# Kernel optimization log

Measured on AMD Instinct MI355X. Metric: run time of the kernel, lower is better.

## Reference

```python
import jax, jax.numpy as jnp
import numpy as np

B, L, H, V = 32, 2048, 128, 32000
ALPHA = 0.95
GATE_THRESH = 0.7
LN_EPS = 1e-5
NORM_EPS = 1e-12


def setup_inputs() -> dict:
    key = jax.random.key(0)
    ks = jax.random.split(key, 12)
    s = 0.02
    return {
        "seq": jax.random.randint(ks[0], (B, L), 0, V),
        "embed_w": jax.random.normal(ks[1], (V, H), jnp.float32) * s,
        "ff_w1": jax.random.normal(ks[2], (2 * H, H), jnp.float32) * s,
        "ff_b1": jnp.zeros((2 * H,), jnp.float32),
        "ff_w2": jax.random.normal(ks[3], (H, 2 * H), jnp.float32) * s,
        "ff_b2": jnp.zeros((H,), jnp.float32),
        "ln_g": jnp.ones((H,), jnp.float32),
        "ln_b": jnp.zeros((H,), jnp.float32),
        "kp_w": jax.random.normal(ks[4], (H, H), jnp.float32) * s,
        "rp_w": jax.random.normal(ks[5], (H, H), jnp.float32) * s,
        "rp_b": jnp.zeros((H,), jnp.float32),
        "out_w": jax.random.normal(ks[6], (V, H), jnp.float32) * s,
        "out_b": jnp.zeros((V,), jnp.float32),
    }


def reference(seq, embed_w, ff_w1, ff_b1, ff_w2, ff_b2, ln_g, ln_b,
              kp_w, rp_w, rp_b, out_w, out_b):
    h = embed_w[seq]                                    # (B,L,H)
    ff = jnp.maximum(h @ ff_w1.T + ff_b1, 0.0) @ ff_w2.T + ff_b2
    x = h + ff
    mu = jnp.mean(x, axis=-1, keepdims=True)
    var = jnp.mean((x - mu) ** 2, axis=-1, keepdims=True)
    h = (x - mu) * jax.lax.rsqrt(var + LN_EPS) * ln_g + ln_b

    k_all = jnp.einsum('blh,oh->blo', h, kp_w)          # kp(h), (B,L,H)
    ks_seq = jnp.transpose(k_all[:, :-1, :], (1, 0, 2)) # (L-1,B,H)

    def step(M, k):
        kn = k / jnp.maximum(jnp.linalg.norm(k, axis=-1, keepdims=True), NORM_EPS)
        vp = jnp.einsum('bij,bj->bi', M, kn)
        err = k - vp
        fire = (jnp.linalg.norm(err, axis=-1)
                >= GATE_THRESH * jnp.linalg.norm(k, axis=-1)).astype(k.dtype)
        delta = fire[:, None, None] * err[:, :, None] * kn[:, None, :]
        return M + (1.0 - ALPHA) * delta, None

    M0 = jnp.zeros((B, H, H), h.dtype)
    M, _ = jax.lax.scan(step, M0, ks_seq)

    q = k_all[:, -1, :]                                 # (B,H)
    read = jnp.einsum('bij,bj->bi', M, q)
    r = read @ rp_w.T + rp_b
    return r @ out_w.T + out_b                          # (B,V)
```

## Files before the change

kernel.cpp:

```cpp
#include <hip/hip_runtime.h>
#include <hip/hip_fp16.h>

#define B_  32
#define L_  2048
#define H_  128
#define H2_ 256
#define V_  32000
#define NT_ (B_*L_)
#define TOKS_PER_BLK 64
#define CH_ 32

template<int CTRL, int RMASK>
__device__ __forceinline__ float dpp_add(float x) {
    int v = __builtin_amdgcn_update_dpp(0, __float_as_int(x), CTRL, RMASK, 0xf, true);
    return x + __int_as_float(v);
}
__device__ __forceinline__ float wave_sum63(float x) {
    x = dpp_add<0x111, 0xf>(x);
    x = dpp_add<0x112, 0xf>(x);
    x = dpp_add<0x114, 0xf>(x);
    x = dpp_add<0x118, 0xf>(x);
    x = dpp_add<0x142, 0xa>(x);
    x = dpp_add<0x143, 0xc>(x);
    return x;
}
__device__ __forceinline__ float wave_allsum(float x) {
    x = wave_sum63(x);
    return __int_as_float(__builtin_amdgcn_readlane(__float_as_int(x), 63));
}
__device__ __forceinline__ float pair_sum(float x) {
    int v = __builtin_amdgcn_update_dpp(0, __float_as_int(x), 0xB1, 0xf, 0xf, true);
    return x + __int_as_float(v);
}

__global__ __launch_bounds__(256, 2) void ka_ff_ln_kp(
    const int*   __restrict__ seq,   const float* __restrict__ embed_w,
    const float* __restrict__ ff_w1, const float* __restrict__ ff_b1,
    const float* __restrict__ ff_w2, const float* __restrict__ ff_b2,
    const float* __restrict__ ln_g,  const float* __restrict__ ln_b,
    const float* __restrict__ kp_w,  float* __restrict__ k_all)
{
    __shared__ __half2 w1p[64][256];
    __shared__ float2 h2[128];
    __shared__ float2 y12[256];
    __shared__ float  p_sh[2][2][128];
    __shared__ float2 hln2[128];
    __shared__ float  red_sh[8];

    const int tid  = threadIdx.x;
    const int half = tid >> 7;
    const int i    = tid & 127;
    const int lane = tid & 63;
    const int wave = tid >> 6;

    for (int idx = tid; idx < 64*256; idx += 256) {
        int o = idx >> 6, j2 = idx & 63;
        float2 ab = *(const float2*)(ff_w1 + o*128 + 2*j2);
        w1p[j2][o] = __floats2half2_rn(ab.x, ab.y);
    }
    __half2 w2r[64];
    {
        const float* src = ff_w2 + (size_t)i*H2_ + half*128;
        #pragma unroll
        for (int q4 = 0; q4 < 16; ++q4) {
            float4 a = *(const float4*)(src + q4*8);
            float4 b = *(const float4*)(src + q4*8 + 4);
            w2r[q4*4+0] = __floats2half2_rn(a.x, a.y);
            w2r[q4*4+1] = __floats2half2_rn(a.z, a.w);
            w2r[q4*4+2] = __floats2half2_rn(b.x, b.y);
            w2r[q4*4+3] = __floats2half2_rn(b.z, b.w);
        }
    }
    float kreg[64];
    {
        const float* src = kp_w + (size_t)i*H_ + half*64;
        #pragma unroll
        for (int j4 = 0; j4 < 16; ++j4) {
            float4 v = *(const float4*)(src + j4*4);
            kreg[j4*4+0]=v.x; kreg[j4*4+1]=v.y; kreg[j4*4+2]=v.z; kreg[j4*4+3]=v.w;
        }
    }
    const float b1v = ff_b1[tid];
    const float b2v = ff_b2[i];
    const float gv  = ln_g[i];
    const float bv  = ln_b[i];
    __syncthreads();

    const int base = blockIdx.x * TOKS_PER_BLK;
    for (int it = 0; it < TOKS_PER_BLK; it += 2) {
        const int t0 = base + it;
        if (tid < 64) {
            int tok = tid >> 5;
            int l32 = tid & 31;
            int v   = seq[t0 + tok];
            float4 hv = *(const float4*)(embed_w + (size_t)v*H_ + l32*4);
            ((float*)&h2[l32*4+0])[tok] = hv.x;
            ((float*)&h2[l32*4+1])[tok] = hv.y;
            ((float*)&h2[l32*4+2])[tok] = hv.z;
            ((float*)&h2[l32*4+3])[tok] = hv.w;
        }
        __syncthreads();
        float a0 = b1v, a1 = b1v;
        #pragma unroll
        for (int j2 = 0; j2 < 64; ++j2) {
            __half2 w = w1p[j2][tid];
            float4 hh = *(const float4*)&h2[2*j2];
            float wl = __low2float(w), wh = __high2float(w);
            a0 = fmaf(wl, hh.x, a0); a0 = fmaf(wh, hh.z, a0);
            a1 = fmaf(wl, hh.y, a1); a1 = fmaf(wh, hh.w, a1);
        }
        y12[tid] = make_float2(fmaxf(a0, 0.f), fmaxf(a1, 0.f));
        __syncthreads();
        float c0 = 0.f, c1 = 0.f;
        #pragma unroll
        for (int q = 0; q < 64; ++q) {
            __half2 w = w2r[q];
            float4 yy = *(const float4*)&y12[half*128 + 2*q];
            float wl = __low2float(w), wh = __high2float(w);
            c0 = fmaf(wl, yy.x, c0); c0 = fmaf(wh, yy.z, c0);
            c1 = fmaf(wl, yy.y, c1); c1 = fmaf(wh, yy.w, c1);
        }
        p_sh[half][0][i] = c0;
        p_sh[half][1][i] = c1;
        __syncthreads();
        float x = ((const float*)&h2[i])[half] + p_sh[0][half][i] + p_sh[1][half][i] + b2v;
        {
            float s = x, s2 = x*x;
            #pragma unroll
            for (int m = 1; m <= 32; m <<= 1) {
                s  += __shfl_xor(s,  m);
                s2 += __shfl_xor(s2, m);
            }
            if (lane == 0) { red_sh[wave*2] = s; red_sh[wave*2+1] = s2; }
        }
        __syncthreads();
        float mu  = (red_sh[half*4+0] + red_sh[half*4+2]) * (1.0f/128.0f);
        float ex2 = (red_sh[half*4+1] + red_sh[half*4+3]) * (1.0f/128.0f);
        float var = ex2 - mu*mu;
        float rstd = 1.0f / sqrtf(var + 1e-5f);
        float hln = (x - mu) * rstd * gv + bv;
        ((float*)&hln2[i])[half] = hln;
        __syncthreads();
        float k0 = 0.f, k1 = 0.f;
        #pragma unroll
        for (int jj = 0; jj < 64; ++jj) {
            float2 hh = hln2[half*64 + jj];
            k0 = fmaf(kreg[jj], hh.x, k0);
            k1 = fmaf(kreg[jj], hh.y, k1);
        }
        p_sh[half][0][i] = k0;
        p_sh[half][1][i] = k1;
        __syncthreads();
        if (tid < 128) {
            k_all[(size_t)t0*H_     + i] = p_sh[0][0][i] + p_sh[1][0][i];
            k_all[(size_t)(t0+1)*H_ + i] = p_sh[0][1][i] + p_sh[1][1][i];
        }
    }
}

__global__ __launch_bounds__(256, 1) void kc_scan(
    const float* __restrict__ k_all, const float* __restrict__ rp_w,
    const float* __restrict__ rp_b,  float* __restrict__ r_out)
{
    __shared__ __align__(16) float kch[2][CH_*H_];
    __shared__ __align__(16) float red[2][4];
    __shared__ __align__(16) float read_sh[128];
    __shared__ float pr_sh[2][128];

    const int b    = blockIdx.x;
    const int tid  = threadIdx.x;
    const int lane = tid & 63;
    const int wave = tid >> 6;
    const int half = lane & 1;
    const int r    = wave*32 + (lane >> 1);

    const float* kb = k_all + (size_t)b * (L_*H_);

    float M[64];
    #pragma unroll
    for (int j = 0; j < 64; ++j) M[j] = 0.f;

    #pragma unroll
    for (int jr = 0; jr < 4; ++jr) {
        float4 v = *(const float4*)(kb + jr*1024 + tid*4);
        *(float4*)&kch[0][jr*1024 + tid*4] = v;
    }
    float4 st[4];
    __syncthreads();

    #pragma unroll 1
    for (int t = 0; t < L_-1; ++t) {
        const int c   = t >> 5;
        const int row = t & 31;
        const int buf = c & 1;
        if (row == 0 && c + 1 < L_/CH_) {
            const float* src = kb + (size_t)(c+1)*(CH_*H_);
            #pragma unroll
            for (int jr = 0; jr < 4; ++jr) st[jr] = *(const float4*)(src + jr*1024 + tid*4);
        }
        if (row == 16 && c + 1 < L_/CH_) {
            float* dst = &kch[buf^1][0];
            #pragma unroll
            for (int jr = 0; jr < 4; ++jr) *(float4*)&dst[jr*1024 + tid*4] = st[jr];
        }
        const float* krow = &kch[buf][row*H_];
        float2 kq = *(const float2*)(krow + (lane<<1));
        float nk2 = wave_allsum(fmaf(kq.x, kq.x, kq.y*kq.y));
        float rn  = 1.0f / fmaxf(sqrtf(nk2), 1e-12f);
        float K[64];
        float a0=0.f, a1=0.f, a2=0.f, a3=0.f;
        #pragma unroll
        for (int j4 = 0; j4 < 16; ++j4) {
            float4 kk = *(const float4*)(krow + half*64 + j4*4);
            K[j4*4+0]=kk.x; K[j4*4+1]=kk.y; K[j4*4+2]=kk.z; K[j4*4+3]=kk.w;
            a0 = fmaf(M[j4*4+0], kk.x, a0);
            a1 = fmaf(M[j4*4+1], kk.y, a1);
            a2 = fmaf(M[j4*4+2], kk.z, a2);
            a3 = fmaf(M[j4*4+3], kk.w, a3);
        }
        float vp = pair_sum((a0+a1) + (a2+a3));
        float kr  = krow[r];
        float err = kr - vp*rn;
        float esum = wave_sum63(err*err);
        if (lane == 63) red[t&1][wave] = esum;
        __syncthreads();
        float4 rv = *(const float4*)&red[t&1][0];
        float ne2x2 = (rv.x+rv.y) + (rv.z+rv.w);
        int fire = ne2x2 >= 0.98f * nk2;
        if (__builtin_amdgcn_readfirstlane(fire)) {
            float sc = 0.05f * err * rn;
            #pragma unroll
            for (int j = 0; j < 64; ++j) M[j] = fmaf(sc, K[j], M[j]);
        }
    }

    {
        const float* qrow = &kch[1][31*H_];
        float a0=0.f, a1=0.f, a2=0.f, a3=0.f;
        #pragma unroll
        for (int j4 = 0; j4 < 16; ++j4) {
            float4 kk = *(const float4*)(qrow + half*64 + j4*4);
            a0 = fmaf(M[j4*4+0], kk.x, a0);
            a1 = fmaf(M[j4*4+1], kk.y, a1);
            a2 = fmaf(M[j4*4+2], kk.z, a2);
            a3 = fmaf(M[j4*4+3], kk.w, a3);
        }
        float vq = pair_sum((a0+a1) + (a2+a3));
        if (half == 0) read_sh[r] = vq;
    }
    __syncthreads();
    {
        const int o  = tid & 127;
        const int hf = tid >> 7;
        float acc = 0.f;
        #pragma unroll
        for (int j4 = 0; j4 < 16; ++j4) {
            float4 wv = *(const float4*)(rp_w + (size_t)o*H_ + hf*64 + j4*4);
            float4 rv = *(const float4*)&read_sh[hf*64 + j4*4];
            acc = fmaf(wv.x, rv.x, acc);
            acc = fmaf(wv.y, rv.y, acc);
            acc = fmaf(wv.z, rv.z, acc);
            acc = fmaf(wv.w, rv.w, acc);
        }
        pr_sh[hf][o] = acc;
    }
    __syncthreads();
    if (tid < 128) r_out[b*H_ + tid] = pr_sh[0][tid] + pr_sh[1][tid] + rp_b[tid];
}

__global__ __launch_bounds__(256) void kd_out(
    const float* __restrict__ r_in, const float* __restrict__ out_w,
    const float* __restrict__ out_b, float* __restrict__ out)
{
    __shared__ float r_sh[B_ * H_];
    const int tid = threadIdx.x;
    for (int idx = tid; idx < B_*H_; idx += 256) r_sh[idx] = r_in[idx];
    __syncthreads();
    const int v = blockIdx.x * 256 + tid;
    const float* wrow = out_w + (size_t)v * H_;
    float acc[B_];
    #pragma unroll
    for (int bb = 0; bb < B_; ++bb) acc[bb] = 0.f;
    for (int h4 = 0; h4 < H_/4; ++h4) {
        float4 w = *(const float4*)(wrow + h4*4);
        #pragma unroll
        for (int bb = 0; bb < B_; ++bb) {
            const float* rr = &r_sh[bb*H_ + h4*4];
            acc[bb] = fmaf(w.x, rr[0], acc[bb]);
            acc[bb] = fmaf(w.y, rr[1], acc[bb]);
            acc[bb] = fmaf(w.z, rr[2], acc[bb]);
            acc[bb] = fmaf(w.w, rr[3], acc[bb]);
        }
    }
    const float bias = out_b[v];
    #pragma unroll
    for (int bb = 0; bb < B_; ++bb) out[(size_t)bb*V_ + v] = acc[bb] + bias;
}

extern "C" void kernel_launch(void* const* d_in, const int* in_sizes, int n_in,
                              void* d_out, int out_size, void* d_ws, size_t ws_size,
                              hipStream_t stream)
{
    const int*   seq     = (const int*)  d_in[0];
    const float* embed_w = (const float*)d_in[1];
    const float* ff_w1   = (const float*)d_in[2];
    const float* ff_b1   = (const float*)d_in[3];
    const float* ff_w2   = (const float*)d_in[4];
    const float* ff_b2   = (const float*)d_in[5];
    const float* ln_g    = (const float*)d_in[6];
    const float* ln_b    = (const float*)d_in[7];
    const float* kp_w    = (const float*)d_in[8];
    const float* rp_w    = (const float*)d_in[9];
    const float* rp_b    = (const float*)d_in[10];
    const float* out_w   = (const float*)d_in[11];
    const float* out_b   = (const float*)d_in[12];
    float* out = (float*)d_out;

    float* k_all = (float*)d_ws;
    float* r_buf = k_all + (size_t)NT_ * H_;

    ka_ff_ln_kp<<<dim3(NT_/TOKS_PER_BLK), dim3(256), 0, stream>>>(
        seq, embed_w, ff_w1, ff_b1, ff_w2, ff_b2, ln_g, ln_b, kp_w, k_all);
    kc_scan<<<dim3(B_), dim3(256), 0, stream>>>(k_all, rp_w, rp_b, r_buf);
    kd_out<<<dim3(V_/256), dim3(256), 0, stream>>>(r_buf, out_w, out_b, out);
}
```

Measured before the change: 1.938 ms.

## Restructure scan with lagged rank-1 update and fdot2 FFN matvecs

The scan loop is restructured so that each step applies the previous step's rank-1 update to M while computing M·k for the next key. The current prediction is corrected algebraically using the dot product between consecutive keys, which removes the separate update pass and the data dependency from the serial critical path. The chunk prefetch and store are rescheduled, and the per-column half rotation is meant to reduce LDS bank conflicts. The feed-forward kernel switches to packed fp16 activations with the fdot2 builtin, which cuts instruction count but adds rounding of activations to half precision.

Result: slower. 2.171 ms (+12.0%).

```diff
diff --git a/kernel.cpp b/kernel.cpp
--- a/kernel.cpp
+++ b/kernel.cpp
@@ -10,6 +10,16 @@
 #define TOKS_PER_BLK 64
 #define CH_ 32
 
+typedef _Float16 h2v __attribute__((ext_vector_type(2)));
+
+__device__ __forceinline__ float fdot2f(h2v a, h2v b, float c) {
+#if __has_builtin(__builtin_amdgcn_fdot2)
+    return __builtin_amdgcn_fdot2(a, b, c, false);
+#else
+    return fmaf((float)a[1], (float)b[1], fmaf((float)a[0], (float)b[0], c));
+#endif
+}
+
 template<int CTRL, int RMASK>
 __device__ __forceinline__ float dpp_add(float x) {
     int v = __builtin_amdgcn_update_dpp(0, __float_as_int(x), CTRL, RMASK, 0xf, true);
@@ -40,9 +50,10 @@
     const float* __restrict__ ln_g,  const float* __restrict__ ln_b,
     const float* __restrict__ kp_w,  float* __restrict__ k_all)
 {
-    __shared__ __half2 w1p[64][256];
+    __shared__ h2v w1p[64][256];
     __shared__ float2 h2[128];
-    __shared__ float2 y12[256];
+    __shared__ h2v   h16[2][64];
+    __shared__ _Float16 y16[2][256];
     __shared__ float  p_sh[2][2][128];
     __shared__ float2 hln2[128];
     __shared__ float  red_sh[8];
@@ -56,19 +67,17 @@
     for (int idx = tid; idx < 64*256; idx += 256) {
         int o = idx >> 6, j2 = idx & 63;
         float2 ab = *(const float2*)(ff_w1 + o*128 + 2*j2);
-        w1p[j2][o] = __floats2half2_rn(ab.x, ab.y);
-    }
-    __half2 w2r[64];
+        h2v p; p[0] = (_Float16)ab.x; p[1] = (_Float16)ab.y;
+        w1p[j2][o] = p;
+    }
+    h2v w2r[64];
     {
         const float* src = ff_w2 + (size_t)i*H2_ + half*128;
         #pragma unroll
-        for (int q4 = 0; q4 < 16; ++q4) {
-            float4 a = *(const float4*)(src + q4*8);
-            float4 b = *(const float4*)(src + q4*8 + 4);
-            w2r[q4*4+0] = __floats2half2_rn(a.x, a.y);
-            w2r[q4*4+1] = __floats2half2_rn(a.z, a.w);
-            w2r[q4*4+2] = __floats2half2_rn(b.x, b.y);
-            w2r[q4*4+3] = __floats2half2_rn(b.z, b.w);
+        for (int q2 = 0; q2 < 64; ++q2) {
+            float2 ab = *(const float2*)(src + 2*q2);
+            h2v p; p[0] = (_Float16)ab.x; p[1] = (_Float16)ab.y;
+            w2r[q2] = p;
         }
     }
     float kreg[64];
@@ -98,27 +107,28 @@
             ((float*)&h2[l32*4+1])[tok] = hv.y;
             ((float*)&h2[l32*4+2])[tok] = hv.z;
             ((float*)&h2[l32*4+3])[tok] = hv.w;
+            h2v pa; pa[0]=(_Float16)hv.x; pa[1]=(_Float16)hv.y;
+            h2v pb; pb[0]=(_Float16)hv.z; pb[1]=(_Float16)hv.w;
+            h16[tok][l32*2+0] = pa;
+            h16[tok][l32*2+1] = pb;
         }
         __syncthreads();
         float a0 = b1v, a1 = b1v;
         #pragma unroll
         for (int j2 = 0; j2 < 64; ++j2) {
-            __half2 w = w1p[j2][tid];
-            float4 hh = *(const float4*)&h2[2*j2];
-            float wl = __low2float(w), wh = __high2float(w);
-            a0 = fmaf(wl, hh.x, a0); a0 = fmaf(wh, hh.z, a0);
-            a1 = fmaf(wl, hh.y, a1); a1 = fmaf(wh, hh.w, a1);
-        }
-        y12[tid] = make_float2(fmaxf(a0, 0.f), fmaxf(a1, 0.f));
+            h2v w = w1p[j2][tid];
+            a0 = fdot2f(w, h16[0][j2], a0);
+            a1 = fdot2f(w, h16[1][j2], a1);
+        }
+        y16[0][tid] = (_Float16)fmaxf(a0, 0.f);
+        y16[1][tid] = (_Float16)fmaxf(a1, 0.f);
         __syncthreads();
         float c0 = 0.f, c1 = 0.f;
         #pragma unroll
-        for (int q = 0; q < 64; ++q) {
-            __half2 w = w2r[q];
-            float4 yy = *(const float4*)&y12[half*128 + 2*q];
-            float wl = __low2float(w), wh = __high2float(w);
-            c0 = fmaf(wl, yy.x, c0); c0 = fmaf(wh, yy.z, c0);
-            c1 = fmaf(wl, yy.y, c1); c1 = fmaf(wh, yy.w, c1);
+        for (int q2 = 0; q2 < 64; ++q2) {
+            h2v w = w2r[q2];
+            c0 = fdot2f(w, *(const h2v*)&y16[0][half*128 + 2*q2], c0);
+            c1 = fdot2f(w, *(const h2v*)&y16[1][half*128 + 2*q2], c1);
         }
         p_sh[half][0][i] = c0;
         p_sh[half][1][i] = c1;
@@ -173,6 +183,8 @@
     const int wave = tid >> 6;
     const int half = lane & 1;
     const int r    = wave*32 + (lane >> 1);
+    const int cbase = half*64;
+    const int jrot  = half*4;
 
     const float* kb = k_all + (size_t)b * (L_*H_);
 
@@ -185,68 +197,76 @@
         float4 v = *(const float4*)(kb + jr*1024 + tid*4);
         *(float4*)&kch[0][jr*1024 + tid*4] = v;
     }
+    __syncthreads();
+
+    float2 kqo = *(const float2*)(kch[0] + (lane<<1));
+    float nk2_cur = wave_allsum(fmaf(kqo.x, kqo.x, kqo.y*kqo.y));
+    float rn_cur  = 1.0f / fmaxf(sqrtf(nk2_cur), 1e-12f);
+    float kr_cur  = kch[0][r];
+    float Q = 0.f, corr = 0.f, upd = 0.f, errprev = 0.f;
     float4 st[4];
-    __syncthreads();
 
     #pragma unroll 1
     for (int t = 0; t < L_-1; ++t) {
-        const int c   = t >> 5;
         const int row = t & 31;
-        const int buf = c & 1;
-        if (row == 0 && c + 1 < L_/CH_) {
-            const float* src = kb + (size_t)(c+1)*(CH_*H_);
-            #pragma unroll
-            for (int jr = 0; jr < 4; ++jr) st[jr] = *(const float4*)(src + jr*1024 + tid*4);
-        }
-        if (row == 16 && c + 1 < L_/CH_) {
+        const int buf = (t>>5) & 1;
+        const int tp  = (t == 0) ? 0 : t - 1;
+        const float* krp = &kch[(tp>>5)&1][(tp&31)*H_];
+        const float* krn = &kch[((t+1)>>5)&1][((t+1)&31)*H_];
+
+        float P   = fmaf(corr, errprev, Q);
+        float err = fmaf(-rn_cur, P, kr_cur);
+        float esum = wave_sum63(err*err);
+        if (lane == 63) red[t&1][wave] = esum;
+
+        float2 kqn = *(const float2*)(krn + (lane<<1));
+        float kr_next = krn[r];
+        float nk2_next = wave_allsum(fmaf(kqn.x, kqn.x, kqn.y*kqn.y));
+        float kap      = wave_allsum(fmaf(kqo.x, kqn.x, kqo.y*kqn.y));
+        float rn_next  = 1.0f / fmaxf(sqrtf(nk2_next), 1e-12f);
+
+        if (row == 17 && t < 2016) {
             float* dst = &kch[buf^1][0];
             #pragma unroll
             for (int jr = 0; jr < 4; ++jr) *(float4*)&dst[jr*1024 + tid*4] = st[jr];
         }
-        const float* krow = &kch[buf][row*H_];
-        float2 kq = *(const float2*)(krow + (lane<<1));
-        float nk2 = wave_allsum(fmaf(kq.x, kq.x, kq.y*kq.y));
-        float rn  = 1.0f / fmaxf(sqrtf(nk2), 1e-12f);
-        float K[64];
-        float a0=0.f, a1=0.f, a2=0.f, a3=0.f;
+
+        float q0=0.f, q1=0.f, q2=0.f, q3=0.f;
         #pragma unroll
         for (int j4 = 0; j4 < 16; ++j4) {
-            float4 kk = *(const float4*)(krow + half*64 + j4*4);
-            K[j4*4+0]=kk.x; K[j4*4+1]=kk.y; K[j4*4+2]=kk.z; K[j4*4+3]=kk.w;
-            a0 = fmaf(M[j4*4+0], kk.x, a0);
-            a1 = fmaf(M[j4*4+1], kk.y, a1);
-            a2 = fmaf(M[j4*4+2], kk.z, a2);
-            a3 = fmaf(M[j4*4+3], kk.w, a3);
-        }
-        float vp = pair_sum((a0+a1) + (a2+a3));
-        float kr  = krow[r];
-        float err = kr - vp*rn;
-        float esum = wave_sum63(err*err);
-        if (lane == 63) red[t&1][wave] = esum;
-        __syncthreads();
+            const int off = cbase + (((j4 + jrot) & 15) << 2);
+            float4 kp = *(const float4*)(krp + off);
+            float4 kn = *(const float4*)(krn + off);
+            M[j4*4+0] = fmaf(upd, kp.x, M[j4*4+0]); q0 = fmaf(M[j4*4+0], kn.x, q0);
+            M[j4*4+1] = fmaf(upd, kp.y, M[j4*4+1]); q1 = fmaf(M[j4*4+1], kn.y, q1);
+            M[j4*4+2] = fmaf(upd, kp.z, M[j4*4+2]); q2 = fmaf(M[j4*4+2], kn.z, q2);
+            M[j4*4+3] = fmaf(upd, kp.w, M[j4*4+3]); q3 = fmaf(M[j4*4+3], kn.w, q3);
+        }
+        float Qn = pair_sum((q0+q1) + (q2+q3));
+
+        __syncthreads();
+
+        if (row == 1 && t < 2016) {
+            const float* src = kb + (size_t)((t>>5)+1)*(CH_*H_);
+            #pragma unroll
+            for (int jr = 0; jr < 4; ++jr) st[jr] = *(const float4*)(src + jr*1024 + tid*4);
+        }
+
         float4 rv = *(const float4*)&red[t&1][0];
-        float ne2x2 = (rv.x+rv.y) + (rv.z+rv.w);
-        int fire = ne2x2 >= 0.98f * nk2;
-        if (__builtin_amdgcn_readfirstlane(fire)) {
-            float sc = 0.05f * err * rn;
-            #pragma unroll
-            for (int j = 0; j < 64; ++j) M[j] = fmaf(sc, K[j], M[j]);
-        }
+        float rsum = (rv.x+rv.y) + (rv.z+rv.w);
+        float c = (rsum >= 0.98f * nk2_cur) ? 0.05f * rn_cur : 0.0f;
+
+        corr = c * kap;
+        upd  = c * err;
+        errprev = err;
+        Q = Qn;
+        nk2_cur = nk2_next; rn_cur = rn_next;
+        kr_cur = kr_next;   kqo = kqn;
     }
 
     {
-        const float* qrow = &kch[1][31*H_];
-        float a0=0.f, a1=0.f, a2=0.f, a3=0.f;
-        #pragma unroll
-        for (int j4 = 0; j4 < 16; ++j4) {
-            float4 kk = *(const float4*)(qrow + half*64 + j4*4);
-            a0 = fmaf(M[j4*4+0], kk.x, a0);
-            a1 = fmaf(M[j4*4+1], kk.y, a1);
-            a2 = fmaf(M[j4*4+2], kk.z, a2);
-            a3 = fmaf(M[j4*4+3], kk.w, a3);
-        }
-        float vq = pair_sum((a0+a1) + (a2+a3));
-        if (half == 0) read_sh[r] = vq;
+        float rdv = fmaf(corr, errprev, Q);
+        if (half == 0) read_sh[r] = rdv;
     }
     __syncthreads();
     {
```

## Software-pipeline scan: fuse rank-1 update with next-step matvec, branchless gate

Applied to the files above, without the earlier changes.

Restructures the sequential memory scan so each iteration applies the previous step's rank-1 update to M and computes the next key's matvec in the same unrolled loop. The fire gate becomes a branchless scale factor, which removes the divergent branch and the separate update pass. Column offsets are rotated by half-wave to avoid LDS bank conflicts, and krow[r] is fetched with ds_bpermute instead of a scalar LDS read. The last iteration's matvec doubles as the final query read. Risks include higher register pressure from holding KT alongside M, and the update FMAs now run even on steps that do not fire.

Result: slower. 1.991 ms (+2.7%).

```diff
diff --git a/kernel.cpp b/kernel.cpp
--- a/kernel.cpp
+++ b/kernel.cpp
@@ -173,6 +173,9 @@
     const int wave = tid >> 6;
     const int half = lane & 1;
     const int r    = wave*32 + (lane >> 1);
+    const int cbase = half*64;
+    const int jrot  = half*4;
+    const int paddr = (r >> 1) << 2;
 
     const float* kb = k_all + (size_t)b * (L_*H_);
 
@@ -185,69 +188,79 @@
         float4 v = *(const float4*)(kb + jr*1024 + tid*4);
         *(float4*)&kch[0][jr*1024 + tid*4] = v;
     }
+    __syncthreads();
+
+    float KT[64];
+    #pragma unroll
+    for (int j4 = 0; j4 < 16; ++j4) {
+        const int off = cbase + (((j4 + jrot) & 15) << 2);
+        float4 kk = *(const float4*)(kch[0] + off);
+        KT[j4*4+0]=kk.x; KT[j4*4+1]=kk.y; KT[j4*4+2]=kk.z; KT[j4*4+3]=kk.w;
+    }
+    float nk2, rn, err;
+    {
+        float2 kq = *(const float2*)(kch[0] + (lane<<1));
+        nk2 = wave_allsum(fmaf(kq.x, kq.x, kq.y*kq.y));
+        rn  = 1.0f / fmaxf(sqrtf(nk2), 1e-12f);
+        float vx = __int_as_float(__builtin_amdgcn_ds_bpermute(paddr, __float_as_int(kq.x)));
+        float vy = __int_as_float(__builtin_amdgcn_ds_bpermute(paddr, __float_as_int(kq.y)));
+        err = (r & 1) ? vy : vx;
+        float es = wave_sum63(err*err);
+        if (lane == 63) red[0][wave] = es;
+    }
+    __syncthreads();
+
+    float Qn = 0.f;
     float4 st[4];
-    __syncthreads();
 
     #pragma unroll 1
-    for (int t = 0; t < L_-1; ++t) {
-        const int c   = t >> 5;
-        const int row = t & 31;
-        const int buf = c & 1;
-        if (row == 0 && c + 1 < L_/CH_) {
-            const float* src = kb + (size_t)(c+1)*(CH_*H_);
+    for (int i = 0; i < L_-1; ++i) {
+        const int tn = i + 1;
+        const float* krn = &kch[(tn>>5)&1][(tn&31)*H_];
+
+        float4 rv = *(const float4*)&red[i&1][0];
+        float rsum = (rv.x+rv.y) + (rv.z+rv.w);
+        float c   = (rsum >= 0.98f * nk2) ? 0.05f : 0.0f;
+        float upd = c * err * rn;
+
+        if ((i & 31) == 1 && i < 2016) {
+            const float* src = kb + (size_t)((i>>5)+1)*(CH_*H_);
             #pragma unroll
             for (int jr = 0; jr < 4; ++jr) st[jr] = *(const float4*)(src + jr*1024 + tid*4);
         }
-        if (row == 16 && c + 1 < L_/CH_) {
-            float* dst = &kch[buf^1][0];
+        if ((i & 31) == 17 && i < 2016) {
+            float* dst = &kch[((i>>5)&1)^1][0];
             #pragma unroll
             for (int jr = 0; jr < 4; ++jr) *(float4*)&dst[jr*1024 + tid*4] = st[jr];
         }
-        const float* krow = &kch[buf][row*H_];
-        float2 kq = *(const float2*)(krow + (lane<<1));
-        float nk2 = wave_allsum(fmaf(kq.x, kq.x, kq.y*kq.y));
-        float rn  = 1.0f / fmaxf(sqrtf(nk2), 1e-12f);
-        float K[64];
-        float a0=0.f, a1=0.f, a2=0.f, a3=0.f;
+
+        float2 kqn = *(const float2*)(krn + (lane<<1));
+        float nk2n = wave_allsum(fmaf(kqn.x, kqn.x, kqn.y*kqn.y));
+        float rnn  = 1.0f / fmaxf(sqrtf(nk2n), 1e-12f);
+        float vx = __int_as_float(__builtin_amdgcn_ds_bpermute(paddr, __float_as_int(kqn.x)));
+        float vy = __int_as_float(__builtin_amdgcn_ds_bpermute(paddr, __float_as_int(kqn.y)));
+        float krr = (r & 1) ? vy : vx;
+
+        float q0=0.f, q1=0.f, q2=0.f, q3=0.f;
         #pragma unroll
         for (int j4 = 0; j4 < 16; ++j4) {
-            float4 kk = *(const float4*)(krow + half*64 + j4*4);
-            K[j4*4+0]=kk.x; K[j4*4+1]=kk.y; K[j4*4+2]=kk.z; K[j4*4+3]=kk.w;
-            a0 = fmaf(M[j4*4+0], kk.x, a0);
-            a1 = fmaf(M[j4*4+1], kk.y, a1);
-            a2 = fmaf(M[j4*4+2], kk.z, a2);
-            a3 = fmaf(M[j4*4+3], kk.w, a3);
-        }
-        float vp = pair_sum((a0+a1) + (a2+a3));
-        float kr  = krow[r];
-        float err = kr - vp*rn;
-        float esum = wave_sum63(err*err);
-        if (lane == 63) red[t&1][wave] = esum;
-        __syncthreads();
-        float4 rv = *(const float4*)&red[t&1][0];
-        float ne2x2 = (rv.x+rv.y) + (rv.z+rv.w);
-        int fire = ne2x2 >= 0.98f * nk2;
-        if (__builtin_amdgcn_readfirstlane(fire)) {
-            float sc = 0.05f * err * rn;
-            #pragma unroll
-            for (int j = 0; j < 64; ++j) M[j] = fmaf(sc, K[j], M[j]);
-        }
-    }
-
-    {
-        const float* qrow = &kch[1][31*H_];
-        float a0=0.f, a1=0.f, a2=0.f, a3=0.f;
-        #pragma unroll
-        for (int j4 = 0; j4 < 16; ++j4) {
-            float4 kk = *(const float4*)(qrow + half*64 + j4*4);
-            a0 = fmaf(M[j4*4+0], kk.x, a0);
-            a1 = fmaf(M[j4*4+1], kk.y, a1);
-            a2 = fmaf(M[j4*4+2], kk.z, a2);
-            a3 = fmaf(M[j4*4+3], kk.w, a3);
-        }
-        float vq = pair_sum((a0+a1) + (a2+a3));
-        if (half == 0) read_sh[r] = vq;
-    }
+            const int off = cbase + (((j4 + jrot) & 15) << 2);
+            float4 kk = *(const float4*)(krn + off);
+            M[j4*4+0] = fmaf(upd, KT[j4*4+0], M[j4*4+0]); q0 = fmaf(M[j4*4+0], kk.x, q0); KT[j4*4+0] = kk.x;
+            M[j4*4+1] = fmaf(upd, KT[j4*4+1], M[j4*4+1]); q1 = fmaf(M[j4*4+1], kk.y, q1); KT[j4*4+1] = kk.y;
+            M[j4*4+2] = fmaf(upd, KT[j4*4+2], M[j4*4+2]); q2 = fmaf(M[j4*4+2], kk.z, q2); KT[j4*4+2] = kk.z;
+            M[j4*4+3] = fmaf(upd, KT[j4*4+3], M[j4*4+3]); q3 = fmaf(M[j4*4+3], kk.w, q3); KT[j4*4+3] = kk.w;
+        }
+        Qn = pair_sum((q0+q1) + (q2+q3));
+
+        err = fmaf(-rnn, Qn, krr);
+        float es = wave_sum63(err*err);
+        if (lane == 63) red[(i+1)&1][wave] = es;
+        nk2 = nk2n; rn = rnn;
+        __syncthreads();
+    }
+
+    if (half == 0) read_sh[r] = Qn;
     __syncthreads();
     {
         const int o  = tid & 127;
```

## Chunk the delta-rule scan into windows with Gram-matrix correction and rank-32 updates

Applied to the files above, without the earlier changes.

The sequential per-token scan is replaced by a windowed scheme over 32-token chunks. For each window it precomputes M·k for all tokens and the window Gram matrix K·K^T in parallel. A single wave then resolves the intra-window dependencies using the Gram matrix and the scaled errors of earlier tokens. M is updated once per window as a rank-32 outer-product accumulation, which removes the per-token block barrier and moves most of the work into parallel matmul-like loops. The block grows to 512 threads, which adds a serial triangular solve on one wave and changes floating-point summation order.

Measured after the change: 1.932 ms. About the same (-0.3%).

```diff
diff --git a/kernel.cpp b/kernel.cpp
--- a/kernel.cpp
+++ b/kernel.cpp
@@ -8,7 +8,8 @@
 #define V_  32000
 #define NT_ (B_*L_)
 #define TOKS_PER_BLK 64
-#define CH_ 32
+#define W_  32
+#define NW_ (L_/W_)
 
 template<int CTRL, int RMASK>
 __device__ __forceinline__ float dpp_add(float x) {
@@ -28,9 +29,18 @@
     x = wave_sum63(x);
     return __int_as_float(__builtin_amdgcn_readlane(__float_as_int(x), 63));
 }
-__device__ __forceinline__ float pair_sum(float x) {
+__device__ __forceinline__ float quad_sum(float x) {
     int v = __builtin_amdgcn_update_dpp(0, __float_as_int(x), 0xB1, 0xf, 0xf, true);
+    x += __int_as_float(v);
+    v = __builtin_amdgcn_update_dpp(0, __float_as_int(x), 0x4E, 0xf, 0xf, true);
     return x + __int_as_float(v);
+}
+__device__ __forceinline__ float sum16_hi(float x) {
+    x = dpp_add<0x111, 0xf>(x);
+    x = dpp_add<0x112, 0xf>(x);
+    x = dpp_add<0x114, 0xf>(x);
+    x = dpp_add<0x118, 0xf>(x);
+    return x;
 }
 
 __global__ __launch_bounds__(256, 2) void ka_ff_ln_kp(
@@ -158,109 +168,161 @@
     }
 }
 
-__global__ __launch_bounds__(256, 1) void kc_scan(
+__global__ __launch_bounds__(512, 2) void kc_scan(
     const float* __restrict__ k_all, const float* __restrict__ rp_w,
     const float* __restrict__ rp_b,  float* __restrict__ r_out)
 {
-    __shared__ __align__(16) float kch[2][CH_*H_];
-    __shared__ __align__(16) float red[2][4];
-    __shared__ __align__(16) float read_sh[128];
-    __shared__ float pr_sh[2][128];
+    __shared__ __align__(16) float kch[2][W_*H_];
+    __shared__ __align__(16) float P_lds[W_][H_];
+    __shared__ __align__(16) float G_T[W_][34];
+    __shared__ __align__(16) float escT[H_][34];
+    __shared__ __align__(16) float read_sh[H_];
+    __shared__ float pr_sh[2][H_];
 
     const int b    = blockIdx.x;
     const int tid  = threadIdx.x;
     const int lane = tid & 63;
-    const int wave = tid >> 6;
-    const int half = lane & 1;
-    const int r    = wave*32 + (lane >> 1);
+    const int wv   = tid >> 6;
+    const int r    = tid >> 2;
+    const int s    = tid & 3;
+    const int cb   = s << 5;
+    const int gi   = tid >> 4;
+    const int gc   = (tid & 15) << 3;
 
     const float* kb = k_all + (size_t)b * (L_*H_);
 
-    float M[64];
+    float Mreg[32];
     #pragma unroll
-    for (int j = 0; j < 64; ++j) M[j] = 0.f;
-
-    #pragma unroll
-    for (int jr = 0; jr < 4; ++jr) {
-        float4 v = *(const float4*)(kb + jr*1024 + tid*4);
-        *(float4*)&kch[0][jr*1024 + tid*4] = v;
-    }
-    float4 st[4];
+    for (int m = 0; m < 32; ++m) Mreg[m] = 0.f;
+
+    {
+        float4 a = *(const float4*)(kb + tid*8);
+        float4 c = *(const float4*)(kb + tid*8 + 4);
+        *(float4*)&kch[0][tid*8]     = a;
+        *(float4*)&kch[0][tid*8 + 4] = c;
+    }
     __syncthreads();
 
     #pragma unroll 1
-    for (int t = 0; t < L_-1; ++t) {
-        const int c   = t >> 5;
-        const int row = t & 31;
-        const int buf = c & 1;
-        if (row == 0 && c + 1 < L_/CH_) {
-            const float* src = kb + (size_t)(c+1)*(CH_*H_);
+    for (int w = 0; w < NW_; ++w) {
+        const int buf = w & 1;
+        const float* kcur = kch[buf];
+        const float* kprv = kch[buf^1];
+
+        float4 st0, st1;
+        if (w + 1 < NW_) {
+            const float* src = kb + (size_t)(w+1)*(W_*H_) + tid*8;
+            st0 = *(const float4*)(src);
+            st1 = *(const float4*)(src + 4);
+        }
+
+        if (w > 0) {
             #pragma unroll
-            for (int jr = 0; jr < 4; ++jr) st[jr] = *(const float4*)(src + jr*1024 + tid*4);
-        }
-        if (row == 16 && c + 1 < L_/CH_) {
-            float* dst = &kch[buf^1][0];
+            for (int j2 = 0; j2 < 16; ++j2) {
+                float2 e2 = *(const float2*)&escT[r][2*j2];
+                const float* ka0 = kprv + (2*j2)*H_ + cb;
+                const float* ka1 = kprv + (2*j2+1)*H_ + cb;
+                #pragma unroll
+                for (int m8 = 0; m8 < 8; ++m8) {
+                    const int a = ((m8 + 2*s) & 7) << 2;
+                    float4 kv0 = *(const float4*)(ka0 + a);
+                    float4 kv1 = *(const float4*)(ka1 + a);
+                    Mreg[m8*4+0] = fmaf(e2.x, kv0.x, Mreg[m8*4+0]);
+                    Mreg[m8*4+1] = fmaf(e2.x, kv0.y, Mreg[m8*4+1]);
+                    Mreg[m8*4+2] = fmaf(e2.x, kv0.z, Mreg[m8*4+2]);
+                    Mreg[m8*4+3] = fmaf(e2.x, kv0.w, Mreg[m8*4+3]);
+                    Mreg[m8*4+0] = fmaf(e2.y, kv1.x, Mreg[m8*4+0]);
+                    Mreg[m8*4+1] = fmaf(e2.y, kv1.y, Mreg[m8*4+1]);
+                    Mreg[m8*4+2] = fmaf(e2.y, kv1.z, Mreg[m8*4+2]);
+                    Mreg[m8*4+3] = fmaf(e2.y, kv1.w, Mreg[m8*4+3]);
+                }
+            }
+        }
+        __syncthreads();
+
+        if (w + 1 < NW_) {
+            *(float4*)&kch[buf^1][tid*8]     = st0;
+            *(float4*)&kch[buf^1][tid*8 + 4] = st1;
+        }
+
+        {
+            float4 kia = *(const float4*)(kcur + gi*H_ + gc);
+            float4 kib = *(const float4*)(kcur + gi*H_ + gc + 4);
             #pragma unroll
-            for (int jr = 0; jr < 4; ++jr) *(float4*)&dst[jr*1024 + tid*4] = st[jr];
-        }
-        const float* krow = &kch[buf][row*H_];
-        float2 kq = *(const float2*)(krow + (lane<<1));
-        float nk2 = wave_allsum(fmaf(kq.x, kq.x, kq.y*kq.y));
-        float rn  = 1.0f / fmaxf(sqrtf(nk2), 1e-12f);
-        float K[64];
-        float a0=0.f, a1=0.f, a2=0.f, a3=0.f;
-        #pragma unroll
-        for (int j4 = 0; j4 < 16; ++j4) {
-            float4 kk = *(const float4*)(krow + half*64 + j4*4);
-            K[j4*4+0]=kk.x; K[j4*4+1]=kk.y; K[j4*4+2]=kk.z; K[j4*4+3]=kk.w;
-            a0 = fmaf(M[j4*4+0], kk.x, a0);
-            a1 = fmaf(M[j4*4+1], kk.y, a1);
-            a2 = fmaf(M[j4*4+2], kk.z, a2);
-            a3 = fmaf(M[j4*4+3], kk.w, a3);
-        }
-        float vp = pair_sum((a0+a1) + (a2+a3));
-        float kr  = krow[r];
-        float err = kr - vp*rn;
-        float esum = wave_sum63(err*err);
-        if (lane == 63) red[t&1][wave] = esum;
-        __syncthreads();
-        float4 rv = *(const float4*)&red[t&1][0];
-        float ne2x2 = (rv.x+rv.y) + (rv.z+rv.w);
-        int fire = ne2x2 >= 0.98f * nk2;
-        if (__builtin_amdgcn_readfirstlane(fire)) {
-            float sc = 0.05f * err * rn;
+            for (int j = 0; j < W_; ++j) {
+                const float* kj = kcur + j*H_;
+                float p0=0.f, p1=0.f, p2=0.f, p3=0.f;
+                #pragma unroll
+                for (int m8 = 0; m8 < 8; ++m8) {
+                    const int a = ((m8 + 2*s) & 7) << 2;
+                    float4 kv = *(const float4*)(kj + cb + a);
+                    p0 = fmaf(Mreg[m8*4+0], kv.x, p0);
+                    p1 = fmaf(Mreg[m8*4+1], kv.y, p1);
+                    p2 = fmaf(Mreg[m8*4+2], kv.z, p2);
+                    p3 = fmaf(Mreg[m8*4+3], kv.w, p3);
+                }
+                float p = quad_sum((p0+p1) + (p2+p3));
+                if (s == 0) P_lds[j][r] = p;
+                float4 ga = *(const float4*)(kj + gc);
+                float4 gb = *(const float4*)(kj + gc + 4);
+                float g0 = kia.x*ga.x + kia.y*ga.y;
+                g0 = fmaf(kia.z, ga.z, g0); g0 = fmaf(kia.w, ga.w, g0);
+                float g1 = kib.x*gb.x + kib.y*gb.y;
+                g1 = fmaf(kib.z, gb.z, g1); g1 = fmaf(kib.w, gb.w, g1);
+                float g = sum16_hi(g0 + g1);
+                if ((tid & 15) == 15) G_T[j][gi] = g;
+            }
+        }
+        __syncthreads();
+
+        if (wv == 0) {
+            const int last = (w == NW_-1);
             #pragma unroll
-            for (int j = 0; j < 64; ++j) M[j] = fmaf(sc, K[j], M[j]);
-        }
-    }
-
-    {
-        const float* qrow = &kch[1][31*H_];
-        float a0=0.f, a1=0.f, a2=0.f, a3=0.f;
-        #pragma unroll
-        for (int j4 = 0; j4 < 16; ++j4) {
-            float4 kk = *(const float4*)(qrow + half*64 + j4*4);
-            a0 = fmaf(M[j4*4+0], kk.x, a0);
-            a1 = fmaf(M[j4*4+1], kk.y, a1);
-            a2 = fmaf(M[j4*4+2], kk.z, a2);
-            a3 = fmaf(M[j4*4+3], kk.w, a3);
-        }
-        float vq = pair_sum((a0+a1) + (a2+a3));
-        if (half == 0) read_sh[r] = vq;
-    }
-    __syncthreads();
-    {
+            for (int j = 0; j < W_; ++j) {
+                float nk2 = G_T[j][j];
+                float rn  = 1.0f / fmaxf(sqrtf(nk2), 1e-12f);
+                float t0 = P_lds[j][lane];
+                float t1 = P_lds[j][lane + 64];
+                float k0 = kcur[j*H_ + lane];
+                float k1 = kcur[j*H_ + 64 + lane];
+                #pragma unroll
+                for (int i2 = 0; i2 < ((j+1)>>1); ++i2) {
+                    float2 g2 = *(const float2*)&G_T[j][2*i2];
+                    float2 ea = *(const float2*)&escT[lane][2*i2];
+                    float2 eb = *(const float2*)&escT[lane+64][2*i2];
+                    t0 = fmaf(g2.x, ea.x, t0); t1 = fmaf(g2.x, eb.x, t1);
+                    if (2*i2+1 < j) {
+                        t0 = fmaf(g2.y, ea.y, t0); t1 = fmaf(g2.y, eb.y, t1);
+                    }
+                }
+                if (last && j == W_-1) {
+                    read_sh[lane]      = t0;
+                    read_sh[lane + 64] = t1;
+                } else {
+                    float e0 = fmaf(-rn, t0, k0);
+                    float e1 = fmaf(-rn, t1, k1);
+                    float es = wave_allsum(fmaf(e0, e0, e1*e1));
+                    float sc = (es >= 0.49f * nk2) ? 0.05f * rn : 0.f;
+                    escT[lane][j]      = sc * e0;
+                    escT[lane + 64][j] = sc * e1;
+                }
+            }
+        }
+        __syncthreads();
+    }
+
+    if (tid < 256) {
         const int o  = tid & 127;
         const int hf = tid >> 7;
         float acc = 0.f;
         #pragma unroll
         for (int j4 = 0; j4 < 16; ++j4) {
-            float4 wv = *(const float4*)(rp_w + (size_t)o*H_ + hf*64 + j4*4);
-            float4 rv = *(const float4*)&read_sh[hf*64 + j4*4];
-            acc = fmaf(wv.x, rv.x, acc);
-            acc = fmaf(wv.y, rv.y, acc);
-            acc = fmaf(wv.z, rv.z, acc);
-            acc = fmaf(wv.w, rv.w, acc);
+            float4 wvv = *(const float4*)(rp_w + (size_t)o*H_ + hf*64 + j4*4);
+            float4 rv  = *(const float4*)&read_sh[hf*64 + j4*4];
+            acc = fmaf(wvv.x, rv.x, acc);
+            acc = fmaf(wvv.y, rv.y, acc);
+            acc = fmaf(wvv.z, rv.z, acc);
+            acc = fmaf(wvv.w, rv.w, acc);
         }
         pr_sh[hf][o] = acc;
     }
@@ -321,6 +383,6 @@
 
     ka_ff_ln_kp<<<dim3(NT_/TOKS_PER_BLK), dim3(256), 0, stream>>>(
         seq, embed_w, ff_w1, ff_b1, ff_w2, ff_b2, ln_g, ln_b, kp_w, k_all);
-    kc_scan<<<dim3(B_), dim3(256), 0, stream>>>(k_all, rp_w, rp_b, r_buf);
+    kc_scan<<<dim3(B_), dim3(512), 0, stream>>>(k_all, rp_w, rp_b, r_buf);
     kd_out<<<dim3(V_/256), dim3(256), 0, stream>>>(r_buf, out_w, out_b, out);
 }
```
